# Kernel optimization log

Hardware: AMD Instinct MI355X
Metric: run time of the kernel (lower is better)

## Reference

```python
import jax, jax.numpy as jnp
import numpy as np

L, B, I, H, O = 8, 1, 2048, 2048, 1000  # num_layers, batch, input, hidden, output


def setup_inputs() -> dict:
    key = jax.random.key(0)
    ks = jax.random.split(key, 20)
    s = 1.0 / np.sqrt(H)  # torch nn.Linear default init bound

    def w(k, shape):
        return jax.random.uniform(k, shape, jnp.float32, -s, s)

    inp = {
        "x": jax.random.normal(ks[0], (B, 1, I), jnp.float32),
        "h": jax.random.normal(ks[1], (L, B, H), jnp.float32),
    }
    # six gate linears per layer; input_size == hidden_size so all stack to [L, H, H]
    for i, n in enumerate(["W_ir", "W_hr", "W_h1", "W_x1", "W_iu", "W_hu"]):
        inp[n] = w(ks[2 + 2 * i], (L, H, H))
        inp["b" + n[1:]] = w(ks[3 + 2 * i], (L, H))
    inp["W_fc"] = w(ks[14], (O, H))
    inp["b_fc"] = w(ks[15], (O,))
    return inp


def reference(x, h, W_ir, b_ir, W_hr, b_hr, W_h1, b_h1, W_x1, b_x1,
              W_iu, b_iu, W_hu, b_hu, W_fc, b_fc):
    # Layer 0 input is x[:, 0, :]; layer l>0 input is the ORIGINAL h[l-1]
    # (not the freshly computed hidden), so all layers are independent -> batch them.
    inp = jnp.concatenate([x[:, 0, :][None, :, :], h[:-1]], axis=0)  # [L, B, H]

    def lin(v, W, b):  # per-layer torch Linear: v @ W.T + b, batched over L
        return jnp.einsum('lbi,lhi->lbh', v, W) + b[:, None, :]

    reset_gate = jax.nn.sigmoid(lin(inp, W_ir, b_ir) + lin(h, W_hr, b_hr))
    r = jnp.tanh(reset_gate * lin(h, W_h1, b_h1) + lin(inp, W_x1, b_x1))
    update_gate = jax.nn.sigmoid(lin(inp, W_iu, b_iu) + lin(h, W_hu, b_hu))
    new_h = (1.0 - update_gate) * r + update_gate * h  # [L, B, H]

    out = jax.nn.log_softmax(jnp.maximum(new_h[-1], 0.0) @ W_fc.T + b_fc, axis=1)
    return (out, new_h)
```

## Files before the change

### kernel.cpp

```cpp
#include <hip/hip_runtime.h>
#include <math.h>

#define NL 8
#define NH 2048
#define NO 1000

__device__ __forceinline__ float dot4(float4 a, float4 b) {
    return a.x * b.x + a.y * b.y + a.z * b.z + a.w * b.w;
}

__device__ __forceinline__ float4 relu4(float4 a) {
    return make_float4(fmaxf(a.x, 0.f), fmaxf(a.y, 0.f), fmaxf(a.z, 0.f), fmaxf(a.w, 0.f));
}

__device__ __forceinline__ float wave_sum(float v) {
#pragma unroll
    for (int off = 32; off > 0; off >>= 1) v += __shfl_xor(v, off);
    return v;
}

__global__ __launch_bounds__(256) void gru_gates_kernel(
    const float* __restrict__ x,
    const float* __restrict__ h,
    const float* __restrict__ W_ir, const float* __restrict__ b_ir,
    const float* __restrict__ W_hr, const float* __restrict__ b_hr,
    const float* __restrict__ W_h1, const float* __restrict__ b_h1,
    const float* __restrict__ W_x1, const float* __restrict__ b_x1,
    const float* __restrict__ W_iu, const float* __restrict__ b_iu,
    const float* __restrict__ W_hu, const float* __restrict__ b_hu,
    float* __restrict__ new_h)
{
    const int wave = (blockIdx.x * blockDim.x + threadIdx.x) >> 6;
    const int lane = threadIdx.x & 63;
    const int l   = wave >> 11;
    const int row = wave & (NH - 1);

    const float4* __restrict__ vi = (const float4*)((l == 0) ? x : (h + (size_t)(l - 1) * NH));
    const float4* __restrict__ vh = (const float4*)(h + (size_t)l * NH);

    const size_t wbase = ((size_t)l * NH + row) * NH;
    const float4* __restrict__ wir = (const float4*)(W_ir + wbase);
    const float4* __restrict__ whr = (const float4*)(W_hr + wbase);
    const float4* __restrict__ wh1 = (const float4*)(W_h1 + wbase);
    const float4* __restrict__ wx1 = (const float4*)(W_x1 + wbase);
    const float4* __restrict__ wiu = (const float4*)(W_iu + wbase);
    const float4* __restrict__ whu = (const float4*)(W_hu + wbase);

    float s_ir = 0.f, s_hr = 0.f, s_h1 = 0.f, s_x1 = 0.f, s_iu = 0.f, s_hu = 0.f;

#pragma unroll
    for (int it = 0; it < NH / 4 / 64 / 2; ++it) {
        const int k0 = it * 128 + lane;
        const int k1 = k0 + 64;
        const float4 a0   = vi[k0];
        const float4 b0   = vh[k0];
        const float4 t0_ir = wir[k0];
        const float4 t0_hr = whr[k0];
        const float4 t0_h1 = wh1[k0];
        const float4 t0_x1 = wx1[k0];
        const float4 t0_iu = wiu[k0];
        const float4 t0_hu = whu[k0];
        const float4 a1   = vi[k1];
        const float4 b1   = vh[k1];
        const float4 t1_ir = wir[k1];
        const float4 t1_hr = whr[k1];
        const float4 t1_h1 = wh1[k1];
        const float4 t1_x1 = wx1[k1];
        const float4 t1_iu = wiu[k1];
        const float4 t1_hu = whu[k1];
        s_ir += dot4(a0, t0_ir) + dot4(a1, t1_ir);
        s_hr += dot4(b0, t0_hr) + dot4(b1, t1_hr);
        s_h1 += dot4(b0, t0_h1) + dot4(b1, t1_h1);
        s_x1 += dot4(a0, t0_x1) + dot4(a1, t1_x1);
        s_iu += dot4(a0, t0_iu) + dot4(a1, t1_iu);
        s_hu += dot4(b0, t0_hu) + dot4(b1, t1_hu);
    }

    s_ir = wave_sum(s_ir);
    s_hr = wave_sum(s_hr);
    s_h1 = wave_sum(s_h1);
    s_x1 = wave_sum(s_x1);
    s_iu = wave_sum(s_iu);
    s_hu = wave_sum(s_hu);

    if (lane == 0) {
        const int bi = l * NH + row;
        const float dir = s_ir + b_ir[bi];
        const float dhr = s_hr + b_hr[bi];
        const float dh1 = s_h1 + b_h1[bi];
        const float dx1 = s_x1 + b_x1[bi];
        const float diu = s_iu + b_iu[bi];
        const float dhu = s_hu + b_hu[bi];
        const float reset = 1.f / (1.f + expf(-(dir + dhr)));
        const float r     = tanhf(reset * dh1 + dx1);
        const float u     = 1.f / (1.f + expf(-(diu + dhu)));
        const float hv    = h[bi];
        new_h[bi] = (1.f - u) * r + u * hv;
    }
}

__global__ __launch_bounds__(256) void fc_kernel(
    const float* __restrict__ new_h,
    const float* __restrict__ W_fc,
    const float* __restrict__ b_fc,
    float* __restrict__ logits)
{
    const int wave = (blockIdx.x * blockDim.x + threadIdx.x) >> 6;
    const int lane = threadIdx.x & 63;
    if (wave >= NO) return;
    const float4* __restrict__ v = (const float4*)(new_h + (size_t)(NL - 1) * NH);
    const float4* __restrict__ w = (const float4*)(W_fc + (size_t)wave * NH);
    float s = 0.f;
#pragma unroll
    for (int it = 0; it < NH / 4 / 64 / 2; ++it) {
        const int k0 = it * 128 + lane;
        const int k1 = k0 + 64;
        const float4 v0 = v[k0];
        const float4 w0 = w[k0];
        const float4 v1 = v[k1];
        const float4 w1 = w[k1];
        s += dot4(relu4(v0), w0) + dot4(relu4(v1), w1);
    }
    s = wave_sum(s);
    if (lane == 0) logits[wave] = s + b_fc[wave];
}

__global__ __launch_bounds__(1024) void lsm_kernel(
    const float* __restrict__ logits, float* __restrict__ out)
{
    const int t = threadIdx.x;
    const int lane = t & 63;
    const int wid = t >> 6;
    __shared__ float sred[16];

    const float v = (t < NO) ? logits[t] : -INFINITY;

    float m = v;
#pragma unroll
    for (int off = 32; off > 0; off >>= 1) m = fmaxf(m, __shfl_xor(m, off));
    if (lane == 0) sred[wid] = m;
    __syncthreads();
    if (wid == 0) {
        float mm = (t < 16) ? sred[t] : -INFINITY;
#pragma unroll
        for (int off = 8; off > 0; off >>= 1) mm = fmaxf(mm, __shfl_xor(mm, off));
        if (t == 0) sred[0] = mm;
    }
    __syncthreads();
    const float M = sred[0];
    __syncthreads();

    float e = (t < NO) ? expf(v - M) : 0.f;
    float s = e;
#pragma unroll
    for (int off = 32; off > 0; off >>= 1) s += __shfl_xor(s, off);
    if (lane == 0) sred[wid] = s;
    __syncthreads();
    if (wid == 0) {
        float ss = (t < 16) ? sred[t] : 0.f;
#pragma unroll
        for (int off = 8; off > 0; off >>= 1) ss += __shfl_xor(ss, off);
        if (t == 0) sred[0] = ss;
    }
    __syncthreads();
    const float lse = M + logf(sred[0]);

    if (t < NO) out[t] = v - lse;
}

extern "C" void kernel_launch(void* const* d_in, const int* in_sizes, int n_in,
                              void* d_out, int out_size, void* d_ws, size_t ws_size,
                              hipStream_t stream) {
    const float* x    = (const float*)d_in[0];
    const float* h    = (const float*)d_in[1];
    const float* W_ir = (const float*)d_in[2];
    const float* b_ir = (const float*)d_in[3];
    const float* W_hr = (const float*)d_in[4];
    const float* b_hr = (const float*)d_in[5];
    const float* W_h1 = (const float*)d_in[6];
    const float* b_h1 = (const float*)d_in[7];
    const float* W_x1 = (const float*)d_in[8];
    const float* b_x1 = (const float*)d_in[9];
    const float* W_iu = (const float*)d_in[10];
    const float* b_iu = (const float*)d_in[11];
    const float* W_hu = (const float*)d_in[12];
    const float* b_hu = (const float*)d_in[13];
    const float* W_fc = (const float*)d_in[14];
    const float* b_fc = (const float*)d_in[15];

    float* out    = (float*)d_out;
    float* new_h  = out + NO;
    float* logits = (float*)d_ws;

    gru_gates_kernel<<<(NL * NH) / 4, 256, 0, stream>>>(
        x, h, W_ir, b_ir, W_hr, b_hr, W_h1, b_h1, W_x1, b_x1,
        W_iu, b_iu, W_hu, b_hu, new_h);

    fc_kernel<<<(NO + 3) / 4, 256, 0, stream>>>(new_h, W_fc, b_fc, logits);

    lsm_kernel<<<1, 1024, 0, stream>>>(logits, out);
}
```

Baseline: 142.9 us.

## Split GRU gate matvecs across six waves per output row

Each output row now gets its own 384-thread block, and each of its six waves computes one gate's dot product. All eight weight float4 loads are issued up front, and the results are combined through shared memory after a barrier. The aim is more memory-level parallelism and more waves in flight for the bandwidth-bound 400MB weight stream. In exchange the block count grows to 16384, a __syncthreads is added per row, and only one thread does the final nonlinearity.

```diff
diff --git a/kernel.cpp b/kernel.cpp
--- a/kernel.cpp
+++ b/kernel.cpp
@@ -19,7 +19,7 @@
     return v;
 }
 
-__global__ __launch_bounds__(256) void gru_gates_kernel(
+__global__ __launch_bounds__(384) void gru_gates_kernel(
     const float* __restrict__ x,
     const float* __restrict__ h,
     const float* __restrict__ W_ir, const float* __restrict__ b_ir,
@@ -30,70 +30,56 @@
     const float* __restrict__ W_hu, const float* __restrict__ b_hu,
     float* __restrict__ new_h)
 {
-    const int wave = (blockIdx.x * blockDim.x + threadIdx.x) >> 6;
+    const int bi   = blockIdx.x;
+    const int l    = bi >> 11;
+    const int g    = threadIdx.x >> 6;
     const int lane = threadIdx.x & 63;
-    const int l   = wave >> 11;
-    const int row = wave & (NH - 1);
 
-    const float4* __restrict__ vi = (const float4*)((l == 0) ? x : (h + (size_t)(l - 1) * NH));
-    const float4* __restrict__ vh = (const float4*)(h + (size_t)l * NH);
+    __shared__ float part[6];
 
-    const size_t wbase = ((size_t)l * NH + row) * NH;
-    const float4* __restrict__ wir = (const float4*)(W_ir + wbase);
-    const float4* __restrict__ whr = (const float4*)(W_hr + wbase);
-    const float4* __restrict__ wh1 = (const float4*)(W_h1 + wbase);
-    const float4* __restrict__ wx1 = (const float4*)(W_x1 + wbase);
-    const float4* __restrict__ wiu = (const float4*)(W_iu + wbase);
-    const float4* __restrict__ whu = (const float4*)(W_hu + wbase);
+    const float* __restrict__ W;
+    const float* __restrict__ bv;
+    const float* vecf;
+    const float* vi = (l == 0) ? x : (h + (size_t)(l - 1) * NH);
+    const float* vh = h + (size_t)l * NH;
+    switch (g) {
+        case 0:  W = W_ir; bv = b_ir; vecf = vi; break;
+        case 1:  W = W_hr; bv = b_hr; vecf = vh; break;
+        case 2:  W = W_h1; bv = b_h1; vecf = vh; break;
+        case 3:  W = W_x1; bv = b_x1; vecf = vi; break;
+        case 4:  W = W_iu; bv = b_iu; vecf = vi; break;
+        default: W = W_hu; bv = b_hu; vecf = vh; break;
+    }
+    const float4* __restrict__ wrow = (const float4*)(W + (size_t)bi * NH);
+    const float4* __restrict__ vec  = (const float4*)vecf;
 
-    float s_ir = 0.f, s_hr = 0.f, s_h1 = 0.f, s_x1 = 0.f, s_iu = 0.f, s_hu = 0.f;
+    const float4 w0 = wrow[lane +   0];
+    const float4 w1 = wrow[lane +  64];
+    const float4 w2 = wrow[lane + 128];
+    const float4 w3 = wrow[lane + 192];
+    const float4 w4 = wrow[lane + 256];
+    const float4 w5 = wrow[lane + 320];
+    const float4 w6 = wrow[lane + 384];
+    const float4 w7 = wrow[lane + 448];
 
-#pragma unroll
-    for (int it = 0; it < NH / 4 / 64 / 2; ++it) {
-        const int k0 = it * 128 + lane;
-        const int k1 = k0 + 64;
-        const float4 a0   = vi[k0];
-        const float4 b0   = vh[k0];
-        const float4 t0_ir = wir[k0];
-        const float4 t0_hr = whr[k0];
-        const float4 t0_h1 = wh1[k0];
-        const float4 t0_x1 = wx1[k0];
-        const float4 t0_iu = wiu[k0];
-        const float4 t0_hu = whu[k0];
-        const float4 a1   = vi[k1];
-        const float4 b1   = vh[k1];
-        const float4 t1_ir = wir[k1];
-        const float4 t1_hr = whr[k1];
-        const float4 t1_h1 = wh1[k1];
-        const float4 t1_x1 = wx1[k1];
-        const float4 t1_iu = wiu[k1];
-        const float4 t1_hu = whu[k1];
-        s_ir += dot4(a0, t0_ir) + dot4(a1, t1_ir);
-        s_hr += dot4(b0, t0_hr) + dot4(b1, t1_hr);
-        s_h1 += dot4(b0, t0_h1) + dot4(b1, t1_h1);
-        s_x1 += dot4(a0, t0_x1) + dot4(a1, t1_x1);
-        s_iu += dot4(a0, t0_iu) + dot4(a1, t1_iu);
-        s_hu += dot4(b0, t0_hu) + dot4(b1, t1_hu);
-    }
+    float s;
+    s  = dot4(vec[lane +   0], w0);
+    s += dot4(vec[lane +  64], w1);
+    s += dot4(vec[lane + 128], w2);
+    s += dot4(vec[lane + 192], w3);
+    s += dot4(vec[lane + 256], w4);
+    s += dot4(vec[lane + 320], w5);
+    s += dot4(vec[lane + 384], w6);
+    s += dot4(vec[lane + 448], w7);
 
-    s_ir = wave_sum(s_ir);
-    s_hr = wave_sum(s_hr);
-    s_h1 = wave_sum(s_h1);
-    s_x1 = wave_sum(s_x1);
-    s_iu = wave_sum(s_iu);
-    s_hu = wave_sum(s_hu);
+    s = wave_sum(s);
+    if (lane == 0) part[g] = s + bv[bi];
+    __syncthreads();
 
-    if (lane == 0) {
-        const int bi = l * NH + row;
-        const float dir = s_ir + b_ir[bi];
-        const float dhr = s_hr + b_hr[bi];
-        const float dh1 = s_h1 + b_h1[bi];
-        const float dx1 = s_x1 + b_x1[bi];
-        const float diu = s_iu + b_iu[bi];
-        const float dhu = s_hu + b_hu[bi];
-        const float reset = 1.f / (1.f + expf(-(dir + dhr)));
-        const float r     = tanhf(reset * dh1 + dx1);
-        const float u     = 1.f / (1.f + expf(-(diu + dhu)));
+    if (threadIdx.x == 0) {
+        const float reset = 1.f / (1.f + expf(-(part[0] + part[1])));
+        const float r     = tanhf(reset * part[2] + part[3]);
+        const float u     = 1.f / (1.f + expf(-(part[4] + part[5])));
         const float hv    = h[bi];
         new_h[bi] = (1.f - u) * r + u * hv;
     }
@@ -192,7 +178,7 @@
     float* new_h  = out + NO;
     float* logits = (float*)d_ws;
 
-    gru_gates_kernel<<<(NL * NH) / 4, 256, 0, stream>>>(
+    gru_gates_kernel<<<NL * NH, 384, 0, stream>>>(
         x, h, W_ir, b_ir, W_hr, b_hr, W_h1, b_h1, W_x1, b_x1,
         W_iu, b_iu, W_hu, b_hu, new_h);
 
```

Result: no change. 141.4 us (median of 2 runs) (-1.0%).
